# Performance work log

Hardware: AMD Instinct MI355X
Metric: run time of the kernel (lower is better)

The kernel has to match this reference:

```python
import jax, jax.numpy as jnp
import numpy as np

N, T, OBS, ACT, H = 4096, 256, 32, 8, 64
FORGET_BIAS = 1.0


def setup_inputs() -> dict:
    key = jax.random.key(0)
    k1, k2, k3, k4, k5 = jax.random.split(key, 5)
    return {
        "obss": jax.random.normal(k1, (N, T, OBS), dtype=jnp.float32),
        "actions": jax.random.normal(k2, (N, T, ACT), dtype=jnp.float32),
        "W_lstm": jax.random.normal(k3, (OBS + ACT + H, 4 * H), dtype=jnp.float32) * 0.1,
        "b_lstm": jnp.zeros((4 * H,), dtype=jnp.float32),
        "W_dec": jax.random.normal(k4, (H, 1), dtype=jnp.float32),
        "b_dec": jax.random.normal(k5, (1,), dtype=jnp.float32),
    }


def reference(obss, actions, W_lstm, b_lstm, W_dec, b_dec):
    # concat obs+action features: [N, T, OBS+ACT] -> time-major [T, N, D]
    x = jnp.concatenate([obss, actions], axis=-1)
    x = jnp.transpose(x, (1, 0, 2))
    n = x.shape[1]
    c0 = jnp.zeros((n, H), dtype=x.dtype)
    h0 = jnp.zeros((n, H), dtype=x.dtype)

    def step(carry, xt):
        c, h = carry
        # TF BasicLSTMCell: gates ordered i, j (candidate), f, o
        gates = jnp.concatenate([xt, h], axis=1) @ W_lstm + b_lstm
        i, j, f, o = jnp.split(gates, 4, axis=1)
        new_c = c * jax.nn.sigmoid(f + FORGET_BIAS) + jax.nn.sigmoid(i) * jnp.tanh(j)
        new_h = jnp.tanh(new_c) * jax.nn.sigmoid(o)
        return (new_c, new_h), new_h

    _, hs = jax.lax.scan(step, (c0, h0), x)  # hs: [T, N, H]
    # per-timestep linear decode: [T, N, 1]
    out = hs @ W_dec + b_dec
    return out
```

## Files before the change

kernel.cpp:

```cpp
#include <hip/hip_runtime.h>
#include <cstddef>

#define T_STEPS 256
#define OBS     32
#define ACTD    8
#define NB      16
#define HPAD2   152
#define NSEQ    4096

typedef _Float16 f16x8 __attribute__((ext_vector_type(8)));
typedef _Float16 f16x4 __attribute__((ext_vector_type(4)));
typedef _Float16 f16x2 __attribute__((ext_vector_type(2)));
typedef float    f32x4 __attribute__((ext_vector_type(4)));

union F8 { f16x8 v; _Float16 e[8]; f16x2 h2[4]; };
union F4 { f16x4 v; _Float16 e[4]; f16x2 h2[2]; };

#define LOG2E 1.44269504088896f

__device__ __forceinline__ f16x2 pkrtz(float a, float b) {
    return __builtin_bit_cast(f16x2, __builtin_amdgcn_cvt_pkrtz(a, b));
}

__global__ __launch_bounds__(512)
void lstm_fused(const float* __restrict__ obss, const float* __restrict__ actions,
                const float* __restrict__ W, const float* __restrict__ b,
                const float* __restrict__ Wdec, const float* __restrict__ bdec_p,
                float* __restrict__ out)
{
    __shared__ __align__(16) _Float16 Bop[2][NB * HPAD2];
    __shared__ __align__(16) float partb[2][16][20];

    const int tid  = threadIdx.x;
    const int w8   = tid >> 6;
    const int w    = w8 & 3;
    const bool isA = w8 < 4;
    const int lane = tid & 63;
    const int g    = lane >> 4;
    const int m    = lane & 15;
    const int n0   = blockIdx.x * NB;
    const int u0   = 16 * w + 4 * g;
    const int sigb = 32 * (w >> 1) + 8 * g + 4 * (w & 1);

    f16x8 AW[4][4];
    f32x4 wdv = {0.f, 0.f, 0.f, 0.f};
    if (isA) {
        const float* Wc = W + 16 * w + m;
#pragma unroll
        for (int e = 0; e < 4; e++) {
#pragma unroll
            for (int c = 0; c < 2; c++) {
                F8 hi;
#pragma unroll
                for (int i = 0; i < 8; i++) {
                    int k = 32 * c + 16 * (i >> 2) + 4 * g + (i & 3);
                    hi.e[i] = (_Float16)Wc[(40 + k) * 256 + 64 * e];
                }
                AW[e][c] = hi.v;
            }
            F8 xo, xA;
            float bv = b[64 * e + 16 * w + m] + (e == 2 ? 1.0f : 0.0f);
#pragma unroll
            for (int i = 0; i < 8; i++) {
                int kk = 16 * (i >> 2) + 4 * g + (i & 3);
                xo.e[i] = (_Float16)Wc[kk * 256 + 64 * e];
                xA.e[i] = (kk < ACTD) ? (_Float16)Wc[(OBS + kk) * 256 + 64 * e]
                        : (kk == 16)  ? (_Float16)bv
                                      : (_Float16)0.0f;
            }
            AW[e][2] = xo.v;
            AW[e][3] = xA.v;
        }
        wdv = *(const f32x4*)&Wdec[u0];
    }
    const float bd = bdec_p[0];

    for (int i = tid; i < 2 * NB * HPAD2; i += 512)
        (&Bop[0][0])[i] = (_Float16)0.0f;
    __syncthreads();
    if (tid < 32)
        Bop[tid >> 4][(tid & 15) * HPAD2 + 100] = (_Float16)1.0f;

    const float* pO = obss    + ((size_t)(n0 + m) * T_STEPS) * OBS  + 4 * g;
    const float* pA = actions + ((size_t)(n0 + m) * T_STEPS) * ACTD + 4 * g;
    f32x4 xo0 = {0,0,0,0}, xo1 = {0,0,0,0}, xa = {0,0,0,0};
    auto loadx = [&]() {
        xo0 = *(const f32x4*)pO;
        xo1 = *(const f32x4*)(pO + 16);
        pO += OBS;
        if (g < 2) { xa = *(const f32x4*)pA; pA += ACTD; }
    };
    f16x8 bxo;
    f16x4 uaq;
    auto cvtx = [&]() {
        F8 uo;
        uo.h2[0] = pkrtz(xo0[0], xo0[1]);
        uo.h2[1] = pkrtz(xo0[2], xo0[3]);
        uo.h2[2] = pkrtz(xo1[0], xo1[1]);
        uo.h2[3] = pkrtz(xo1[2], xo1[3]);
        F4 ua_;
        ua_.h2[0] = pkrtz(xa[0], xa[1]);
        ua_.h2[1] = pkrtz(xa[2], xa[3]);
        bxo = uo.v;
        uaq = ua_.v;
    };
    auto stagex = [&](int buf) {
        _Float16* xp = &Bop[buf][m * HPAD2 + 64];
        *(f16x8*)(xp + 8 * g) = bxo;
        if (g < 2) *(f16x4*)(xp + 32 + 8 * g) = uaq;
    };

    if (!isA) {
        loadx();
        cvtx();
        stagex(0);
        loadx();
    }
    f32x4 cr = {0.f, 0.f, 0.f, 0.f};
    float* pOut = out + (size_t)((w + 3) & 3) * NSEQ + n0 + lane;

    __syncthreads();
    if (isA) __builtin_amdgcn_s_setprio(1);

#pragma unroll 2
    for (int t = 0; t < T_STEPS; ++t) {
        const int cb  = t & 1;
        const int nb2 = cb ^ 1;
        asm volatile("s_waitcnt lgkmcnt(0)\n\ts_barrier" ::: "memory");

        if (isA) {
            const _Float16* bp = &Bop[cb][m * HPAD2];
            f16x8 f0 = *(const f16x8*)(bp + 8 * g);
            f16x8 f1 = *(const f16x8*)(bp + 32 + 8 * g);
            f16x8 f2 = *(const f16x8*)(bp + 64 + 8 * g);
            f16x8 f3 = *(const f16x8*)(bp + 96 + 8 * g);

            f32x4 acc[4];
#pragma unroll
            for (int e = 0; e < 4; e++) {
                const f32x4 z = {0.f, 0.f, 0.f, 0.f};
                f32x4 aA = __builtin_amdgcn_mfma_f32_16x16x32_f16(AW[e][2], f2, z, 0, 0, 0);
                f32x4 aB = __builtin_amdgcn_mfma_f32_16x16x32_f16(AW[e][3], f3, z, 0, 0, 0);
                aA = __builtin_amdgcn_mfma_f32_16x16x32_f16(AW[e][0], f0, aA, 0, 0, 0);
                aB = __builtin_amdgcn_mfma_f32_16x16x32_f16(AW[e][1], f1, aB, 0, 0, 0);
                acc[e] = aA + aB;
            }

            float h4[4];
#pragma unroll
            for (int r = 0; r < 4; r++) {
                float ef = __builtin_amdgcn_exp2f(acc[2][r] * -LOG2E);
                float ei = __builtin_amdgcn_exp2f(acc[0][r] * -LOG2E);
                float ej = __builtin_amdgcn_exp2f(acc[1][r] * (-2.0f * LOG2E));
                float Fv = 1.0f + ef, Av = 1.0f + ei, Bv = 1.0f + ej;
                float AB = Av * Bv;
                float num = fmaf(cr[r], AB, Fv * (Bv - 2.0f));
                float c = num * __builtin_amdgcn_rcpf(Fv * AB);
                cr[r] = c;
                float ec = __builtin_amdgcn_exp2f(c * (-2.0f * LOG2E));
                float eo = __builtin_amdgcn_exp2f(acc[3][r] * -LOG2E);
                float Dv = 1.0f + ec, Ev = 1.0f + eo;
                h4[r] = (Dv - 2.0f) * __builtin_amdgcn_rcpf(Dv * Ev);
            }
            F4 hi_;
            hi_.h2[0] = pkrtz(h4[0], h4[1]);
            hi_.h2[1] = pkrtz(h4[2], h4[3]);
            *(f16x4*)(&Bop[nb2][m * HPAD2 + sigb]) = hi_.v;

            float p = h4[0] * wdv[0];
            p = fmaf(h4[1], wdv[1], p);
            p = fmaf(h4[2], wdv[2], p);
            p = fmaf(h4[3], wdv[3], p);
            partb[cb][m][4 * w + g] = p;
        } else {
            if (t + 1 < T_STEPS) {
                cvtx();
                stagex(nb2);
            }
            if (t + 2 < T_STEPS) loadx();

            if (t > 0 && w == (t & 3) && lane < 16) {
                const float* pp = &partb[nb2][lane][0];
                f32x4 q0 = *(const f32x4*)pp;
                f32x4 q1 = *(const f32x4*)(pp + 4);
                f32x4 q2 = *(const f32x4*)(pp + 8);
                f32x4 q3 = *(const f32x4*)(pp + 12);
                f32x4 s4 = (q0 + q1) + (q2 + q3);
                *pOut = s4[0] + s4[1] + s4[2] + s4[3] + bd;
                pOut += 4 * NSEQ;
            }
        }
    }
    if (isA) __builtin_amdgcn_s_setprio(0);

    __syncthreads();
    if (!isA && w == 0 && lane < 16) {
        const float* pp = &partb[1][lane][0];
        f32x4 q0 = *(const f32x4*)pp;
        f32x4 q1 = *(const f32x4*)(pp + 4);
        f32x4 q2 = *(const f32x4*)(pp + 8);
        f32x4 q3 = *(const f32x4*)(pp + 12);
        f32x4 s4 = (q0 + q1) + (q2 + q3);
        *pOut = s4[0] + s4[1] + s4[2] + s4[3] + bd;
    }
}

extern "C" void kernel_launch(void* const* d_in, const int* in_sizes, int n_in,
                              void* d_out, int out_size, void* d_ws, size_t ws_size,
                              hipStream_t stream) {
    (void)in_sizes; (void)n_in; (void)d_ws; (void)ws_size; (void)out_size;
    const float* obss    = (const float*)d_in[0];
    const float* actions = (const float*)d_in[1];
    const float* W       = (const float*)d_in[2];
    const float* b       = (const float*)d_in[3];
    const float* Wdec    = (const float*)d_in[4];
    const float* bdec    = (const float*)d_in[5];
    float* out = (float*)d_out;
    lstm_fused<<<dim3(NSEQ / NB), dim3(512), 0, stream>>>(obss, actions, W, b, Wdec, bdec, out);
}
```

Measured before the change: 133.8 us.

## Split LSTM cell update across both wave groups and precompute input projection MFMAs

Moves the input-projection MFMAs (x·W part) for the next step into the tail of the current step, so the critical path at the start of each step only has the two recurrent MFMAs per gate. Half of the per-element cell updates (rows 2,3) are handed to the previously idle loader waves through a new shared-memory accumulator buffer, with an extra barrier per step. The decode partial sums grow to 32 entries per row to cover both groups. This adds a second barrier and LDS traffic per timestep in exchange for halving the transcendental work on the compute waves.

Result: slower. 173.5 us (+29.7%).

```diff
diff --git a/kernel.cpp b/kernel.cpp
--- a/kernel.cpp
+++ b/kernel.cpp
@@ -20,6 +20,22 @@
 
 __device__ __forceinline__ f16x2 pkrtz(float a, float b) {
     return __builtin_bit_cast(f16x2, __builtin_amdgcn_cvt_pkrtz(a, b));
+}
+
+__device__ __forceinline__ float cell_update(float gi, float gj, float gf, float go,
+                                             float& cr) {
+    float ef = __builtin_amdgcn_exp2f(gf * -LOG2E);
+    float ei = __builtin_amdgcn_exp2f(gi * -LOG2E);
+    float ej = __builtin_amdgcn_exp2f(gj * (-2.0f * LOG2E));
+    float Fv = 1.0f + ef, Av = 1.0f + ei, Bv = 1.0f + ej;
+    float AB = Av * Bv;
+    float num = fmaf(cr, AB, Fv * (Bv - 2.0f));
+    float c = num * __builtin_amdgcn_rcpf(Fv * AB);
+    cr = c;
+    float ec = __builtin_amdgcn_exp2f(c * (-2.0f * LOG2E));
+    float eo = __builtin_amdgcn_exp2f(go * -LOG2E);
+    float Dv = 1.0f + ec, Ev = 1.0f + eo;
+    return (Dv - 2.0f) * __builtin_amdgcn_rcpf(Dv * Ev);
 }
 
 __global__ __launch_bounds__(512)
@@ -29,7 +45,8 @@
                 float* __restrict__ out)
 {
     __shared__ __align__(16) _Float16 Bop[2][NB * HPAD2];
-    __shared__ __align__(16) float partb[2][16][20];
+    __shared__ __align__(16) float partb[2][16][36];
+    __shared__ __align__(16) float accbuf[4][4][16][12];
 
     const int tid  = threadIdx.x;
     const int w8   = tid >> 6;
@@ -43,7 +60,6 @@
     const int sigb = 32 * (w >> 1) + 8 * g + 4 * (w & 1);
 
     f16x8 AW[4][4];
-    f32x4 wdv = {0.f, 0.f, 0.f, 0.f};
     if (isA) {
         const float* Wc = W + 16 * w + m;
 #pragma unroll
@@ -71,8 +87,8 @@
             AW[e][2] = xo.v;
             AW[e][3] = xA.v;
         }
-        wdv = *(const f32x4*)&Wdec[u0];
-    }
+    }
+    f32x4 wdv = *(const f32x4*)&Wdec[u0];
     const float bd = bdec_p[0];
 
     for (int i = tid; i < 2 * NB * HPAD2; i += 512)
@@ -116,11 +132,24 @@
         stagex(0);
         loadx();
     }
-    f32x4 cr = {0.f, 0.f, 0.f, 0.f};
+    float crA0 = 0.f, crA1 = 0.f;
+    float crB2 = 0.f, crB3 = 0.f;
     float* pOut = out + (size_t)((w + 3) & 3) * NSEQ + n0 + lane;
 
     __syncthreads();
-    if (isA) __builtin_amdgcn_s_setprio(1);
+
+    f32x4 pP1[4], pP2[4];
+    if (isA) {
+        const _Float16* bq = &Bop[0][m * HPAD2];
+        f16x8 f2 = *(const f16x8*)(bq + 64 + 8 * g);
+        f16x8 f3 = *(const f16x8*)(bq + 96 + 8 * g);
+        const f32x4 z = {0.f, 0.f, 0.f, 0.f};
+#pragma unroll
+        for (int e = 0; e < 4; e++) {
+            pP1[e] = __builtin_amdgcn_mfma_f32_16x16x32_f16(AW[e][2], f2, z, 0, 0, 0);
+            pP2[e] = __builtin_amdgcn_mfma_f32_16x16x32_f16(AW[e][3], f3, z, 0, 0, 0);
+        }
+    }
 
 #pragma unroll 2
     for (int t = 0; t < T_STEPS; ++t) {
@@ -129,69 +158,70 @@
         asm volatile("s_waitcnt lgkmcnt(0)\n\ts_barrier" ::: "memory");
 
         if (isA) {
+            __builtin_amdgcn_s_setprio(1);
             const _Float16* bp = &Bop[cb][m * HPAD2];
             f16x8 f0 = *(const f16x8*)(bp + 8 * g);
             f16x8 f1 = *(const f16x8*)(bp + 32 + 8 * g);
-            f16x8 f2 = *(const f16x8*)(bp + 64 + 8 * g);
-            f16x8 f3 = *(const f16x8*)(bp + 96 + 8 * g);
-
             f32x4 acc[4];
 #pragma unroll
             for (int e = 0; e < 4; e++) {
+                f32x4 a1 = __builtin_amdgcn_mfma_f32_16x16x32_f16(AW[e][0], f0, pP1[e], 0, 0, 0);
+                f32x4 a2 = __builtin_amdgcn_mfma_f32_16x16x32_f16(AW[e][1], f1, pP2[e], 0, 0, 0);
+                acc[e] = a1 + a2;
+            }
+            f32x4 t2 = {acc[0][2], acc[1][2], acc[2][2], acc[3][2]};
+            f32x4 t3 = {acc[0][3], acc[1][3], acc[2][3], acc[3][3]};
+            *(f32x4*)&accbuf[w][g][m][0] = t2;
+            *(f32x4*)&accbuf[w][g][m][4] = t3;
+            __builtin_amdgcn_s_setprio(0);
+            asm volatile("s_waitcnt lgkmcnt(0)\n\ts_barrier" ::: "memory");
+
+            float h0 = cell_update(acc[0][0], acc[1][0], acc[2][0], acc[3][0], crA0);
+            float h1 = cell_update(acc[0][1], acc[1][1], acc[2][1], acc[3][1], crA1);
+            *(f16x2*)(&Bop[nb2][m * HPAD2 + sigb]) = pkrtz(h0, h1);
+            partb[cb][m][4 * w + g] = fmaf(h1, wdv[1], h0 * wdv[0]);
+
+            if (t + 1 < T_STEPS) {
+                const _Float16* bq = &Bop[nb2][m * HPAD2];
+                f16x8 f2 = *(const f16x8*)(bq + 64 + 8 * g);
+                f16x8 f3 = *(const f16x8*)(bq + 96 + 8 * g);
                 const f32x4 z = {0.f, 0.f, 0.f, 0.f};
-                f32x4 aA = __builtin_amdgcn_mfma_f32_16x16x32_f16(AW[e][2], f2, z, 0, 0, 0);
-                f32x4 aB = __builtin_amdgcn_mfma_f32_16x16x32_f16(AW[e][3], f3, z, 0, 0, 0);
-                aA = __builtin_amdgcn_mfma_f32_16x16x32_f16(AW[e][0], f0, aA, 0, 0, 0);
-                aB = __builtin_amdgcn_mfma_f32_16x16x32_f16(AW[e][1], f1, aB, 0, 0, 0);
-                acc[e] = aA + aB;
-            }
-
-            float h4[4];
-#pragma unroll
-            for (int r = 0; r < 4; r++) {
-                float ef = __builtin_amdgcn_exp2f(acc[2][r] * -LOG2E);
-                float ei = __builtin_amdgcn_exp2f(acc[0][r] * -LOG2E);
-                float ej = __builtin_amdgcn_exp2f(acc[1][r] * (-2.0f * LOG2E));
-                float Fv = 1.0f + ef, Av = 1.0f + ei, Bv = 1.0f + ej;
-                float AB = Av * Bv;
-                float num = fmaf(cr[r], AB, Fv * (Bv - 2.0f));
-                float c = num * __builtin_amdgcn_rcpf(Fv * AB);
-                cr[r] = c;
-                float ec = __builtin_amdgcn_exp2f(c * (-2.0f * LOG2E));
-                float eo = __builtin_amdgcn_exp2f(acc[3][r] * -LOG2E);
-                float Dv = 1.0f + ec, Ev = 1.0f + eo;
-                h4[r] = (Dv - 2.0f) * __builtin_amdgcn_rcpf(Dv * Ev);
-            }
-            F4 hi_;
-            hi_.h2[0] = pkrtz(h4[0], h4[1]);
-            hi_.h2[1] = pkrtz(h4[2], h4[3]);
-            *(f16x4*)(&Bop[nb2][m * HPAD2 + sigb]) = hi_.v;
-
-            float p = h4[0] * wdv[0];
-            p = fmaf(h4[1], wdv[1], p);
-            p = fmaf(h4[2], wdv[2], p);
-            p = fmaf(h4[3], wdv[3], p);
-            partb[cb][m][4 * w + g] = p;
+#pragma unroll
+                for (int e = 0; e < 4; e++) {
+                    pP1[e] = __builtin_amdgcn_mfma_f32_16x16x32_f16(AW[e][2], f2, z, 0, 0, 0);
+                    pP2[e] = __builtin_amdgcn_mfma_f32_16x16x32_f16(AW[e][3], f3, z, 0, 0, 0);
+                }
+            }
         } else {
             if (t + 1 < T_STEPS) {
                 cvtx();
                 stagex(nb2);
             }
             if (t + 2 < T_STEPS) loadx();
-
             if (t > 0 && w == (t & 3) && lane < 16) {
                 const float* pp = &partb[nb2][lane][0];
                 f32x4 q0 = *(const f32x4*)pp;
                 f32x4 q1 = *(const f32x4*)(pp + 4);
                 f32x4 q2 = *(const f32x4*)(pp + 8);
                 f32x4 q3 = *(const f32x4*)(pp + 12);
-                f32x4 s4 = (q0 + q1) + (q2 + q3);
+                f32x4 q4 = *(const f32x4*)(pp + 16);
+                f32x4 q5 = *(const f32x4*)(pp + 20);
+                f32x4 q6 = *(const f32x4*)(pp + 24);
+                f32x4 q7 = *(const f32x4*)(pp + 28);
+                f32x4 s4 = ((q0 + q1) + (q2 + q3)) + ((q4 + q5) + (q6 + q7));
                 *pOut = s4[0] + s4[1] + s4[2] + s4[3] + bd;
                 pOut += 4 * NSEQ;
             }
+            asm volatile("s_waitcnt lgkmcnt(0)\n\ts_barrier" ::: "memory");
+
+            f32x4 a2v = *(const f32x4*)&accbuf[w][g][m][0];
+            f32x4 a3v = *(const f32x4*)&accbuf[w][g][m][4];
+            float h2 = cell_update(a2v[0], a2v[1], a2v[2], a2v[3], crB2);
+            float h3 = cell_update(a3v[0], a3v[1], a3v[2], a3v[3], crB3);
+            *(f16x2*)(&Bop[nb2][m * HPAD2 + sigb + 2]) = pkrtz(h2, h3);
+            partb[cb][m][16 + 4 * w + g] = fmaf(h3, wdv[3], h2 * wdv[2]);
         }
     }
-    if (isA) __builtin_amdgcn_s_setprio(0);
 
     __syncthreads();
     if (!isA && w == 0 && lane < 16) {
@@ -200,7 +230,11 @@
         f32x4 q1 = *(const f32x4*)(pp + 4);
         f32x4 q2 = *(const f32x4*)(pp + 8);
         f32x4 q3 = *(const f32x4*)(pp + 12);
-        f32x4 s4 = (q0 + q1) + (q2 + q3);
+        f32x4 q4 = *(const f32x4*)(pp + 16);
+        f32x4 q5 = *(const f32x4*)(pp + 20);
+        f32x4 q6 = *(const f32x4*)(pp + 24);
+        f32x4 q7 = *(const f32x4*)(pp + 28);
+        f32x4 s4 = ((q0 + q1) + (q2 + q3)) + ((q4 + q5) + (q6 + q7));
         *pOut = s4[0] + s4[1] + s4[2] + s4[3] + bd;
     }
 }
```

## Precompute next step's input-projection MFMAs off the recurrent critical path

Applied to the files above, without the earlier changes.

Splits the shared operand buffer into a double-buffered hidden-state buffer and a triple-buffered input buffer. The compute waves now run the x·W MFMAs for step t+1 after writing h_t, and feed the results in as accumulators for the next step's h·W MFMAs. This takes half the MFMAs off the serial dependency chain after each barrier. The loader waves stage inputs two steps ahead, and setprio is now applied only around the MFMA blocks. The cost is extra registers for the held partial accumulators and more LDS.

Result: slower. 148.2 us (+10.7%).

```diff
diff --git a/kernel.cpp b/kernel.cpp
--- a/kernel.cpp
+++ b/kernel.cpp
@@ -5,7 +5,8 @@
 #define OBS     32
 #define ACTD    8
 #define NB      16
-#define HPAD2   152
+#define HPADH   72
+#define XPAD    72
 #define NSEQ    4096
 
 typedef _Float16 f16x8 __attribute__((ext_vector_type(8)));
@@ -28,7 +29,8 @@
                 const float* __restrict__ Wdec, const float* __restrict__ bdec_p,
                 float* __restrict__ out)
 {
-    __shared__ __align__(16) _Float16 Bop[2][NB * HPAD2];
+    __shared__ __align__(16) _Float16 Hbuf[2][NB * HPADH];
+    __shared__ __align__(16) _Float16 xb[3][NB * XPAD];
     __shared__ __align__(16) float partb[2][16][20];
 
     const int tid  = threadIdx.x;
@@ -75,11 +77,13 @@
     }
     const float bd = bdec_p[0];
 
-    for (int i = tid; i < 2 * NB * HPAD2; i += 512)
-        (&Bop[0][0])[i] = (_Float16)0.0f;
+    for (int i = tid; i < 2 * NB * HPADH; i += 512)
+        (&Hbuf[0][0])[i] = (_Float16)0.0f;
+    for (int i = tid; i < 3 * NB * XPAD; i += 512)
+        (&xb[0][0])[i] = (_Float16)0.0f;
     __syncthreads();
-    if (tid < 32)
-        Bop[tid >> 4][(tid & 15) * HPAD2 + 100] = (_Float16)1.0f;
+    if (tid < 48)
+        xb[tid >> 4][(tid & 15) * XPAD + 36] = (_Float16)1.0f;
 
     const float* pO = obss    + ((size_t)(n0 + m) * T_STEPS) * OBS  + 4 * g;
     const float* pA = actions + ((size_t)(n0 + m) * T_STEPS) * ACTD + 4 * g;
@@ -104,23 +108,36 @@
         bxo = uo.v;
         uaq = ua_.v;
     };
-    auto stagex = [&](int buf) {
-        _Float16* xp = &Bop[buf][m * HPAD2 + 64];
+    auto stagex = [&](int slot) {
+        _Float16* xp = &xb[slot][m * XPAD];
         *(f16x8*)(xp + 8 * g) = bxo;
         if (g < 2) *(f16x4*)(xp + 32 + 8 * g) = uaq;
     };
 
     if (!isA) {
-        loadx();
-        cvtx();
-        stagex(0);
+        loadx(); cvtx(); stagex(0);
+        loadx(); cvtx(); stagex(1);
         loadx();
     }
     f32x4 cr = {0.f, 0.f, 0.f, 0.f};
     float* pOut = out + (size_t)((w + 3) & 3) * NSEQ + n0 + lane;
 
     __syncthreads();
-    if (isA) __builtin_amdgcn_s_setprio(1);
+
+    f32x4 pP1[4], pP2[4];
+    if (isA) {
+        const _Float16* xq = &xb[0][m * XPAD];
+        f16x8 f2 = *(const f16x8*)(xq + 8 * g);
+        f16x8 f3 = *(const f16x8*)(xq + 32 + 8 * g);
+        const f32x4 z = {0.f, 0.f, 0.f, 0.f};
+#pragma unroll
+        for (int e = 0; e < 4; e++) {
+            pP1[e] = __builtin_amdgcn_mfma_f32_16x16x32_f16(AW[e][2], f2, z, 0, 0, 0);
+            pP2[e] = __builtin_amdgcn_mfma_f32_16x16x32_f16(AW[e][3], f3, z, 0, 0, 0);
+        }
+    }
+    int xsA = 1;
+    int xsB = 2;
 
 #pragma unroll 2
     for (int t = 0; t < T_STEPS; ++t) {
@@ -129,22 +146,18 @@
         asm volatile("s_waitcnt lgkmcnt(0)\n\ts_barrier" ::: "memory");
 
         if (isA) {
-            const _Float16* bp = &Bop[cb][m * HPAD2];
+            const _Float16* bp = &Hbuf[cb][m * HPADH];
             f16x8 f0 = *(const f16x8*)(bp + 8 * g);
             f16x8 f1 = *(const f16x8*)(bp + 32 + 8 * g);
-            f16x8 f2 = *(const f16x8*)(bp + 64 + 8 * g);
-            f16x8 f3 = *(const f16x8*)(bp + 96 + 8 * g);
-
             f32x4 acc[4];
+            __builtin_amdgcn_s_setprio(1);
 #pragma unroll
             for (int e = 0; e < 4; e++) {
-                const f32x4 z = {0.f, 0.f, 0.f, 0.f};
-                f32x4 aA = __builtin_amdgcn_mfma_f32_16x16x32_f16(AW[e][2], f2, z, 0, 0, 0);
-                f32x4 aB = __builtin_amdgcn_mfma_f32_16x16x32_f16(AW[e][3], f3, z, 0, 0, 0);
-                aA = __builtin_amdgcn_mfma_f32_16x16x32_f16(AW[e][0], f0, aA, 0, 0, 0);
-                aB = __builtin_amdgcn_mfma_f32_16x16x32_f16(AW[e][1], f1, aB, 0, 0, 0);
-                acc[e] = aA + aB;
-            }
+                f32x4 a1 = __builtin_amdgcn_mfma_f32_16x16x32_f16(AW[e][0], f0, pP1[e], 0, 0, 0);
+                f32x4 a2 = __builtin_amdgcn_mfma_f32_16x16x32_f16(AW[e][1], f1, pP2[e], 0, 0, 0);
+                acc[e] = a1 + a2;
+            }
+            __builtin_amdgcn_s_setprio(0);
 
             float h4[4];
 #pragma unroll
@@ -165,20 +178,35 @@
             F4 hi_;
             hi_.h2[0] = pkrtz(h4[0], h4[1]);
             hi_.h2[1] = pkrtz(h4[2], h4[3]);
-            *(f16x4*)(&Bop[nb2][m * HPAD2 + sigb]) = hi_.v;
+            *(f16x4*)(&Hbuf[nb2][m * HPADH + sigb]) = hi_.v;
 
             float p = h4[0] * wdv[0];
             p = fmaf(h4[1], wdv[1], p);
             p = fmaf(h4[2], wdv[2], p);
             p = fmaf(h4[3], wdv[3], p);
             partb[cb][m][4 * w + g] = p;
+
+            if (t + 1 < T_STEPS) {
+                const _Float16* xq = &xb[xsA][m * XPAD];
+                xsA = (xsA == 2) ? 0 : xsA + 1;
+                f16x8 f2 = *(const f16x8*)(xq + 8 * g);
+                f16x8 f3 = *(const f16x8*)(xq + 32 + 8 * g);
+                const f32x4 z = {0.f, 0.f, 0.f, 0.f};
+                __builtin_amdgcn_s_setprio(1);
+#pragma unroll
+                for (int e = 0; e < 4; e++) {
+                    pP1[e] = __builtin_amdgcn_mfma_f32_16x16x32_f16(AW[e][2], f2, z, 0, 0, 0);
+                    pP2[e] = __builtin_amdgcn_mfma_f32_16x16x32_f16(AW[e][3], f3, z, 0, 0, 0);
+                }
+                __builtin_amdgcn_s_setprio(0);
+            }
         } else {
-            if (t + 1 < T_STEPS) {
+            if (t + 2 < T_STEPS) {
                 cvtx();
-                stagex(nb2);
-            }
-            if (t + 2 < T_STEPS) loadx();
-
+                stagex(xsB);
+                xsB = (xsB == 2) ? 0 : xsB + 1;
+            }
+            if (t + 3 < T_STEPS) loadx();
             if (t > 0 && w == (t & 3) && lane < 16) {
                 const float* pp = &partb[nb2][lane][0];
                 f32x4 q0 = *(const f32x4*)pp;
@@ -191,7 +219,6 @@
             }
         }
     }
-    if (isA) __builtin_amdgcn_s_setprio(0);
 
     __syncthreads();
     if (!isA && w == 0 && lane < 16) {
```

## Triple-buffer input staging and prefetch x fragments a step ahead

Applied to the files above, without the earlier changes.

Adds a third LDS slot for the staged x inputs so producer waves stage two steps ahead in a rotating ring. Compute waves now load the x MFMA operands for the next step at the end of the current step, taking those LDS reads off the critical path after the barrier. The s_setprio boost for compute waves is also removed. The change costs extra LDS and registers, and the ring indexing must stay in sync between the producer and consumer waves.

New measurement: 138.1 us. 3.2% more time.

```diff
diff --git a/kernel.cpp b/kernel.cpp
--- a/kernel.cpp
+++ b/kernel.cpp
@@ -29,6 +29,7 @@
                 float* __restrict__ out)
 {
     __shared__ __align__(16) _Float16 Bop[2][NB * HPAD2];
+    __shared__ __align__(16) _Float16 xb3[NB * HPAD2];
     __shared__ __align__(16) float partb[2][16][20];
 
     const int tid  = threadIdx.x;
@@ -42,6 +43,10 @@
     const int u0   = 16 * w + 4 * g;
     const int sigb = 32 * (w >> 1) + 8 * g + 4 * (w & 1);
 
+    auto xbase = [&](int slot) -> _Float16* {
+        return (slot == 0) ? &Bop[0][0] : (slot == 1) ? &Bop[1][0] : &xb3[0];
+    };
+
     f16x8 AW[4][4];
     f32x4 wdv = {0.f, 0.f, 0.f, 0.f};
     if (isA) {
@@ -77,9 +82,11 @@
 
     for (int i = tid; i < 2 * NB * HPAD2; i += 512)
         (&Bop[0][0])[i] = (_Float16)0.0f;
+    for (int i = tid; i < NB * HPAD2; i += 512)
+        xb3[i] = (_Float16)0.0f;
     __syncthreads();
-    if (tid < 32)
-        Bop[tid >> 4][(tid & 15) * HPAD2 + 100] = (_Float16)1.0f;
+    if (tid < 48)
+        xbase(tid >> 4)[(tid & 15) * HPAD2 + 100] = (_Float16)1.0f;
 
     const float* pO = obss    + ((size_t)(n0 + m) * T_STEPS) * OBS  + 4 * g;
     const float* pA = actions + ((size_t)(n0 + m) * T_STEPS) * ACTD + 4 * g;
@@ -104,23 +111,30 @@
         bxo = uo.v;
         uaq = ua_.v;
     };
-    auto stagex = [&](int buf) {
-        _Float16* xp = &Bop[buf][m * HPAD2 + 64];
+    auto stagex = [&](int slot) {
+        _Float16* xp = xbase(slot) + m * HPAD2 + 64;
         *(f16x8*)(xp + 8 * g) = bxo;
         if (g < 2) *(f16x4*)(xp + 32 + 8 * g) = uaq;
     };
 
     if (!isA) {
-        loadx();
-        cvtx();
-        stagex(0);
+        loadx(); cvtx(); stagex(0);
+        loadx(); cvtx(); stagex(1);
         loadx();
     }
     f32x4 cr = {0.f, 0.f, 0.f, 0.f};
     float* pOut = out + (size_t)((w + 3) & 3) * NSEQ + n0 + lane;
 
     __syncthreads();
-    if (isA) __builtin_amdgcn_s_setprio(1);
+
+    f16x8 f2, f3;
+    if (isA) {
+        const _Float16* xq = &Bop[0][0] + m * HPAD2 + 64;
+        f2 = *(const f16x8*)(xq + 8 * g);
+        f3 = *(const f16x8*)(xq + 32 + 8 * g);
+    }
+    int xsA = 1;
+    int xsB = 2;
 
 #pragma unroll 2
     for (int t = 0; t < T_STEPS; ++t) {
@@ -132,8 +146,6 @@
             const _Float16* bp = &Bop[cb][m * HPAD2];
             f16x8 f0 = *(const f16x8*)(bp + 8 * g);
             f16x8 f1 = *(const f16x8*)(bp + 32 + 8 * g);
-            f16x8 f2 = *(const f16x8*)(bp + 64 + 8 * g);
-            f16x8 f3 = *(const f16x8*)(bp + 96 + 8 * g);
 
             f32x4 acc[4];
 #pragma unroll
@@ -172,13 +184,20 @@
             p = fmaf(h4[2], wdv[2], p);
             p = fmaf(h4[3], wdv[3], p);
             partb[cb][m][4 * w + g] = p;
+
+            if (t + 1 < T_STEPS) {
+                const _Float16* xq = xbase(xsA) + m * HPAD2 + 64;
+                xsA = (xsA == 2) ? 0 : xsA + 1;
+                f2 = *(const f16x8*)(xq + 8 * g);
+                f3 = *(const f16x8*)(xq + 32 + 8 * g);
+            }
         } else {
-            if (t + 1 < T_STEPS) {
+            if (t + 2 < T_STEPS) {
                 cvtx();
-                stagex(nb2);
-            }
-            if (t + 2 < T_STEPS) loadx();
-
+                stagex(xsB);
+                xsB = (xsB == 2) ? 0 : xsB + 1;
+            }
+            if (t + 3 < T_STEPS) loadx();
             if (t > 0 && w == (t & 3) && lane < 16) {
                 const float* pp = &partb[nb2][lane][0];
                 f32x4 q0 = *(const f32x4*)pp;
@@ -191,7 +210,6 @@
             }
         }
     }
-    if (isA) __builtin_amdgcn_s_setprio(0);
 
     __syncthreads();
     if (!isA && w == 0 && lane < 16) {
```
